# Optimization experiments

Hardware: AMD Instinct MI355X
Metric: run time of the kernel (lower is better)

## Reference

```python
import jax, jax.numpy as jnp
import numpy as np

IN_DIM = 128
HID = 128
OUT = 128

def _linear(x, W, b):
    return x @ W + b

def setup_inputs() -> dict:
    key = jax.random.key(0)
    ks = jax.random.split(key, 16)
    B, N = 2, 512
    def w(k, fan_in, fan_out):
        lim = 1.0 / np.sqrt(fan_in)
        return jax.random.uniform(k, (fan_in, fan_out), jnp.float32, -lim, lim)
    def bvec(k, fan_in, fan_out):
        lim = 1.0 / np.sqrt(fan_in)
        return jax.random.uniform(k, (fan_out,), jnp.float32, -lim, lim)
    return {
        "features": jax.random.normal(ks[0], (B, N, IN_DIM), jnp.float32),
        "coords": jax.random.normal(ks[1], (B, N, 3), jnp.float32),
        "eW1": w(ks[2], 2 * IN_DIM + 1, HID), "eb1": bvec(ks[3], 2 * IN_DIM + 1, HID),
        "eW2": w(ks[4], HID, HID), "eb2": bvec(ks[5], HID, HID),
        "nW1": w(ks[6], IN_DIM + HID, HID), "nb1": bvec(ks[7], IN_DIM + HID, HID),
        "nW2": w(ks[8], HID, OUT), "nb2": bvec(ks[9], HID, OUT),
        "cW1": w(ks[10], HID, HID), "cb1": bvec(ks[11], HID, HID),
        "cW2": w(ks[12], HID, 1), "cb2": bvec(ks[13], HID, 1),
    }

def reference(features, coords, eW1, eb1, eW2, eb2, nW1, nb1, nW2, nb2, cW1, cb1, cW2, cb2):
    B, N, D = features.shape
    # pairwise coordinate differences and distances: (B, N, N, 3), (B, N, N, 1)
    coord_diff = coords[:, :, None, :] - coords[:, None, :, :]
    distances = jnp.sqrt(jnp.sum(coord_diff ** 2, axis=-1, keepdims=True) + 1e-8)
    # all-pairs edge features: (B, N, N, 2D+1)
    feat_i = jnp.broadcast_to(features[:, :, None, :], (B, N, N, D))
    feat_j = jnp.broadcast_to(features[:, None, :, :], (B, N, N, D))
    edge_features = jnp.concatenate([feat_i, feat_j, distances], axis=-1)
    edge_hidden = _linear(jax.nn.silu(_linear(edge_features, eW1, eb1)), eW2, eb2)
    # mean over neighbors j -> (B, N, HID)
    aggregated = jnp.mean(edge_hidden, axis=2)
    node_input = jnp.concatenate([features, aggregated], axis=-1)
    updated_features = _linear(jax.nn.silu(_linear(node_input, nW1, nb1)), nW2, nb2)
    # coordinate update
    coord_weights = _linear(jax.nn.silu(_linear(edge_hidden, cW1, cb1)), cW2, cb2)  # (B,N,N,1)
    updated_coords = coords + jnp.mean(coord_weights * coord_diff, axis=2)
    return (updated_features, updated_coords)
```

## Files before the change

### kernel.cpp

```cpp
#include <hip/hip_runtime.h>
#include <hip/hip_bf16.h>
#include <math.h>


typedef float f32x4 __attribute__((ext_vector_type(4)));
typedef short short8 __attribute__((ext_vector_type(8)));

#define MFMA16(a, b, c) __builtin_amdgcn_mfma_f32_16x16x32_bf16((a), (b), (c), 0, 0, 0)

__device__ __forceinline__ short f2bf(float x) {
    __hip_bfloat16 h = __float2bfloat16(x);
    union { __hip_bfloat16 h; short s; } v; v.h = h;
    return v.s;
}
__device__ __forceinline__ float bf2f(short s) {
    union { unsigned u; float f; } v; v.u = ((unsigned)(unsigned short)s) << 16;
    return v.f;
}
__device__ __forceinline__ float silu_f(float x) {
    return x * __builtin_amdgcn_rcpf(1.0f + __expf(-x));
}

__device__ __forceinline__ int swz(int row, int col) {
    int byte = (row << 8) | (col << 1);
    byte ^= (row & 7) << 4;
    return byte >> 1;
}

__global__ void egnn_prew(const float* __restrict__ feat, const float* __restrict__ eW1,
                          const float* __restrict__ eb1,
                          const float* __restrict__ eW2, const float* __restrict__ cW1,
                          const float* __restrict__ eb2, const float* __restrict__ cb1,
                          float* __restrict__ Abuf, float* __restrict__ Bbuf,
                          unsigned short* __restrict__ MbfT, float* __restrict__ bias2ws,
                          float* __restrict__ aggpart, float* __restrict__ coordpart) {
    const int bid = blockIdx.x;
    const int t = threadIdx.x;
    if (bid < 1024) {
        __shared__ float f[128];
        if (t < 128) f[t] = feat[bid * 128 + t];
        __syncthreads();
        const int col  = t & 127;
        const int half = t >> 7;
        const float* W = eW1 + (size_t)half * 128 * 128 + col;
        float acc = half ? 0.f : eb1[col];
        #pragma unroll 8
        for (int k = 0; k < 128; ++k) acc += f[k] * W[(size_t)k * 128];
        if (half == 0) Abuf[bid * 128 + col] = acc;
        else           Bbuf[bid * 128 + col] = acc;
        if (t < 128) aggpart[(size_t)bid * 128 + t] = 0.f;
        if (t < 3)   coordpart[bid * 3 + t] = 0.f;
    } else {
        const int idx = (bid - 1024) * 2 + (t >> 7);
        const int c = t & 127;
        if (idx < 128) {
            float acc = 0.f;
            #pragma unroll 8
            for (int h = 0; h < 128; ++h) acc += eW2[idx * 128 + h] * cW1[h * 128 + c];
            MbfT[c * 128 + idx] = (unsigned short)f2bf(acc);
        } else if (idx == 128) {
            float acc = cb1[c];
            #pragma unroll 8
            for (int h = 0; h < 128; ++h) acc += eb2[h] * cW1[h * 128 + c];
            bias2ws[c] = acc;
        }
    }
}

__global__ void __launch_bounds__(256, 2) egnn_main(
    const float* __restrict__ coords, const float* __restrict__ eW1,
    const float* __restrict__ cW2, const float* __restrict__ cb2,
    const float* __restrict__ Abuf, const float* __restrict__ Bbuf,
    const unsigned short* __restrict__ MbfT, const float* __restrict__ bias2ws,
    float* __restrict__ aggpart, float* __restrict__ coordpart)
{
    constexpr int Nn = 512;
    __shared__ __align__(16) short se[64 * 128];
    __shared__ float aw[128], wd[128];
    __shared__ float cdp[2][3][64];
    __shared__ float warr[2][4][64];
    __shared__ float aggred[16][128];
    __shared__ float cred[4][3];
    __shared__ float ci3[3];

    const int tid  = threadIdx.x;
    const int lane = tid & 63;
    const int wave = tid >> 6;
    const int bid  = blockIdx.x;
    const int node = bid >> 2;
    const int quad = bid & 3;
    const int b    = node >> 9;

    if (tid < 128) {
        aw[tid] = Abuf[node * 128 + tid];
        wd[tid] = eW1[256 * 128 + tid];
    }
    if (tid == 0) {
        ci3[0] = coords[node * 3 + 0];
        ci3[1] = coords[node * 3 + 1];
        ci3[2] = coords[node * 3 + 2];
    }

    const int cfrag = wave * 32 + (lane & 15);
    const int koff  = (lane >> 4) * 8;
    short8 wfM[2][4];
    #pragma unroll
    for (int n2 = 0; n2 < 2; ++n2)
        #pragma unroll
        for (int k = 0; k < 4; ++k)
            wfM[n2][k] = *(const short8*)&MbfT[(size_t)(cfrag + n2 * 16) * 128 + k * 32 + koff];
    __syncthreads();

    const float b2_0  = bias2ws[cfrag], b2_1 = bias2ws[cfrag + 16];
    const float cw2_0 = cW2[cfrag],     cw2_1 = cW2[cfrag + 16];
    const float cb2v  = cb2[0];
    const float cix = ci3[0], ciy = ci3[1], ciz = ci3[2];

    const int jr = tid >> 2, cb = (tid & 3) * 32;
    const int rg = tid >> 4, c8 = (tid & 15) * 8;

    float ap[8];
    #pragma unroll
    for (int q = 0; q < 8; ++q) ap[q] = 0.f;
    float cax = 0.f, cay = 0.f, caz = 0.f;

    for (int t = 0; t < 2; ++t) {
        const int par = t & 1;
        {
            const int j = quad * 128 + t * 64 + jr;
            const float dx = cix - coords[(b * Nn + j) * 3 + 0];
            const float dy = ciy - coords[(b * Nn + j) * 3 + 1];
            const float dz = ciz - coords[(b * Nn + j) * 3 + 2];
            const float dj = sqrtf(dx * dx + dy * dy + dz * dz + 1e-8f);
            if ((tid & 3) == 0) {
                cdp[par][0][jr] = dx; cdp[par][1][jr] = dy; cdp[par][2][jr] = dz;
            }
            const float* Bj = Bbuf + (size_t)(b * Nn + j) * 128 + cb;
            #pragma unroll
            for (int cc = 0; cc < 32; cc += 8) {
                f32x4 x0 = *(const f32x4*)(Bj + cc);
                f32x4 x1 = *(const f32x4*)(Bj + cc + 4);
                short8 v;
                #pragma unroll
                for (int r = 0; r < 4; ++r) {
                    const int c = cb + cc + r;
                    v[r] = f2bf(silu_f(aw[c] + x0[r] + dj * wd[c]));
                }
                #pragma unroll
                for (int r = 0; r < 4; ++r) {
                    const int c = cb + cc + 4 + r;
                    v[4 + r] = f2bf(silu_f(aw[c] + x1[r] + dj * wd[c]));
                }
                *(short8*)&se[swz(jr, cb + cc)] = v;
            }
        }
        __syncthreads();

        f32x4 acc[4][2];
        #pragma unroll
        for (int m = 0; m < 4; ++m) {
            acc[m][0] = (f32x4){b2_0, b2_0, b2_0, b2_0};
            acc[m][1] = (f32x4){b2_1, b2_1, b2_1, b2_1};
        }
        #pragma unroll
        for (int m = 0; m < 4; ++m)
            #pragma unroll
            for (int k = 0; k < 4; ++k) {
                short8 a = *(const short8*)&se[swz(m * 16 + (lane & 15), k * 32 + koff)];
                acc[m][0] = MFMA16(a, wfM[0][k], acc[m][0]);
                acc[m][1] = MFMA16(a, wfM[1][k], acc[m][1]);
            }

        #pragma unroll
        for (int r = 0; r < 4; ++r) {
            short8 v = *(const short8*)&se[swz(rg * 4 + r, c8)];
            #pragma unroll
            for (int q = 0; q < 8; ++q) ap[q] += bf2f(v[q]);
        }

        #pragma unroll
        for (int m = 0; m < 4; ++m)
            #pragma unroll
            for (int reg = 0; reg < 4; ++reg) {
                float v = silu_f(acc[m][0][reg]) * cw2_0
                        + silu_f(acc[m][1][reg]) * cw2_1;
                v += __shfl_xor(v, 1); v += __shfl_xor(v, 2);
                v += __shfl_xor(v, 4); v += __shfl_xor(v, 8);
                if ((lane & 15) == 0)
                    warr[par][wave][m * 16 + (lane >> 4) * 4 + reg] = v;
            }
        __syncthreads();

        if (lane < 16) {
            const int row = wave * 16 + lane;
            const float w = warr[par][0][row] + warr[par][1][row]
                          + warr[par][2][row] + warr[par][3][row] + cb2v;
            cax += w * cdp[par][0][row];
            cay += w * cdp[par][1][row];
            caz += w * cdp[par][2][row];
        }
    }

    #pragma unroll
    for (int q = 0; q < 8; ++q) aggred[rg][c8 + q] = ap[q];
    {
        float sx = cax, sy = cay, sz = caz;
        sx += __shfl_xor(sx, 1); sy += __shfl_xor(sy, 1); sz += __shfl_xor(sz, 1);
        sx += __shfl_xor(sx, 2); sy += __shfl_xor(sy, 2); sz += __shfl_xor(sz, 2);
        sx += __shfl_xor(sx, 4); sy += __shfl_xor(sy, 4); sz += __shfl_xor(sz, 4);
        sx += __shfl_xor(sx, 8); sy += __shfl_xor(sy, 8); sz += __shfl_xor(sz, 8);
        if (lane == 0) { cred[wave][0] = sx; cred[wave][1] = sy; cred[wave][2] = sz; }
    }
    __syncthreads();
    if (tid < 128) {
        float s = 0.f;
        #pragma unroll
        for (int g = 0; g < 16; ++g) s += aggred[g][tid];
        atomicAdd(&aggpart[(size_t)node * 128 + tid], s);
    }
    if (tid < 3) {
        atomicAdd(&coordpart[node * 3 + tid],
                  cred[0][tid] + cred[1][tid] + cred[2][tid] + cred[3][tid]);
    }
}

__global__ void egnn_post(
    const float* __restrict__ features, const float* __restrict__ coords,
    const float* __restrict__ eW2, const float* __restrict__ eb2,
    const float* __restrict__ nW1, const float* __restrict__ nb1,
    const float* __restrict__ nW2, const float* __restrict__ nb2,
    const float* __restrict__ aggpart, const float* __restrict__ coordpart,
    float* __restrict__ out_feat, float* __restrict__ out_coord)
{
    __shared__ float aggs[128], aggh[128], hbuf[128], fi[128], part[128];
    const int node = blockIdx.x;
    const int tid  = threadIdx.x;
    const int c = tid & 127, g = tid >> 7;

    if (tid < 128) {
        aggs[tid] = aggpart[(size_t)node * 128 + tid];
        fi[tid]   = features[node * 128 + tid];
    }
    if (tid < 3)
        out_coord[node * 3 + tid] = coords[node * 3 + tid]
                                  + coordpart[node * 3 + tid] * (1.f / 512.f);
    __syncthreads();
    {
        float acc = 0.f;
        #pragma unroll 8
        for (int k = g * 64; k < g * 64 + 64; ++k) acc += aggs[k] * eW2[k * 128 + c];
        if (g == 1) part[c] = acc;
        __syncthreads();
        if (g == 0) aggh[c] = (acc + part[c]) * (1.f / 512.f) + eb2[c];
        __syncthreads();
    }
    {
        float acc = (g == 0) ? nb1[c] : 0.f;
        const float* src = (g == 0) ? fi : aggh;
        const float* W = nW1 + (size_t)(g << 7) * 128 + c;
        #pragma unroll 8
        for (int k = 0; k < 128; ++k) acc += src[k] * W[(size_t)k * 128];
        if (g == 1) part[c] = acc;
        __syncthreads();
        if (g == 0) hbuf[c] = silu_f(acc + part[c]);
        __syncthreads();
    }
    {
        float acc = (g == 0) ? nb2[c] : 0.f;
        #pragma unroll 8
        for (int k = g * 64; k < g * 64 + 64; ++k) acc += hbuf[k] * nW2[k * 128 + c];
        if (g == 1) part[c] = acc;
        __syncthreads();
        if (g == 0) out_feat[node * 128 + c] = acc + part[c];
    }
}

extern "C" void kernel_launch(void* const* d_in, const int* in_sizes, int n_in,
                              void* d_out, int out_size, void* d_ws, size_t ws_size,
                              hipStream_t stream)
{
    const float* features = (const float*)d_in[0];
    const float* coords   = (const float*)d_in[1];
    const float* eW1 = (const float*)d_in[2];
    const float* eb1 = (const float*)d_in[3];
    const float* eW2 = (const float*)d_in[4];
    const float* eb2 = (const float*)d_in[5];
    const float* nW1 = (const float*)d_in[6];
    const float* nb1 = (const float*)d_in[7];
    const float* nW2 = (const float*)d_in[8];
    const float* nb2 = (const float*)d_in[9];
    const float* cW1 = (const float*)d_in[10];
    const float* cb1 = (const float*)d_in[11];
    const float* cW2 = (const float*)d_in[12];
    const float* cb2 = (const float*)d_in[13];

    float* out = (float*)d_out;
    float* out_feat  = out;
    float* out_coord = out + 2 * 512 * 128;

    float* Abuf      = (float*)d_ws;
    float* Bbuf      = Abuf + 2 * 512 * 128;
    unsigned short* MbfT = (unsigned short*)(Bbuf + 2 * 512 * 128);
    float* bias2ws   = (float*)(MbfT + 128 * 128);
    float* aggpart   = bias2ws + 128;
    float* coordpart = aggpart + 1024 * 128;

    egnn_prew<<<1089, 256, 0, stream>>>(features, eW1, eb1, eW2, cW1, eb2, cb1,
                                        Abuf, Bbuf, MbfT, bias2ws, aggpart, coordpart);
    egnn_main<<<4096, 256, 0, stream>>>(coords, eW1, cW2, cb2,
                                        Abuf, Bbuf, MbfT, bias2ws,
                                        aggpart, coordpart);
    egnn_post<<<1024, 256, 0, stream>>>(features, coords, eW2, eb2,
                                        nW1, nb1, nW2, nb2,
                                        aggpart, coordpart, out_feat, out_coord);
}
```

Baseline: 184.9 us.

## Fuse node-update MLP into main kernel via last-block completion counter

Removes the separate post kernel. Each node is now split across two blocks instead of four, and each block handles 256 neighbours over four tiles. A per-node atomic counter picks the last finishing block, which then reads the accumulated partial sums and runs the node MLP and coordinate update. This saves one kernel launch and halves the number of atomic partial writes. In exchange it adds a threadfence and an atomic handshake, and the tail MLP work now runs unevenly inside the main kernel's blocks.

```diff
diff --git a/kernel.cpp b/kernel.cpp
--- a/kernel.cpp
+++ b/kernel.cpp
@@ -33,7 +33,8 @@
                           const float* __restrict__ eb2, const float* __restrict__ cb1,
                           float* __restrict__ Abuf, float* __restrict__ Bbuf,
                           unsigned short* __restrict__ MbfT, float* __restrict__ bias2ws,
-                          float* __restrict__ aggpart, float* __restrict__ coordpart) {
+                          float* __restrict__ aggpart, float* __restrict__ coordpart,
+                          int* __restrict__ done) {
     const int bid = blockIdx.x;
     const int t = threadIdx.x;
     if (bid < 1024) {
@@ -50,6 +51,7 @@
         else           Bbuf[bid * 128 + col] = acc;
         if (t < 128) aggpart[(size_t)bid * 128 + t] = 0.f;
         if (t < 3)   coordpart[bid * 3 + t] = 0.f;
+        if (t == 0)  done[bid] = 0;
     } else {
         const int idx = (bid - 1024) * 2 + (t >> 7);
         const int c = t & 127;
@@ -68,11 +70,17 @@
 }
 
 __global__ void __launch_bounds__(256, 2) egnn_main(
-    const float* __restrict__ coords, const float* __restrict__ eW1,
+    const float* __restrict__ features, const float* __restrict__ coords,
+    const float* __restrict__ eW1, const float* __restrict__ eW2,
+    const float* __restrict__ eb2,
+    const float* __restrict__ nW1, const float* __restrict__ nb1,
+    const float* __restrict__ nW2, const float* __restrict__ nb2,
     const float* __restrict__ cW2, const float* __restrict__ cb2,
     const float* __restrict__ Abuf, const float* __restrict__ Bbuf,
     const unsigned short* __restrict__ MbfT, const float* __restrict__ bias2ws,
-    float* __restrict__ aggpart, float* __restrict__ coordpart)
+    float* __restrict__ aggpart, float* __restrict__ coordpart,
+    int* __restrict__ done,
+    float* __restrict__ out_feat, float* __restrict__ out_coord)
 {
     constexpr int Nn = 512;
     __shared__ __align__(16) short se[64 * 128];
@@ -82,13 +90,15 @@
     __shared__ float aggred[16][128];
     __shared__ float cred[4][3];
     __shared__ float ci3[3];
+    __shared__ float pfi[128], paggh[128], phbuf[128], ppart[128], pcd[3];
+    __shared__ int lastflag;
 
     const int tid  = threadIdx.x;
     const int lane = tid & 63;
     const int wave = tid >> 6;
     const int bid  = blockIdx.x;
-    const int node = bid >> 2;
-    const int quad = bid & 3;
+    const int node = bid >> 1;
+    const int half = bid & 1;
     const int b    = node >> 9;
 
     if (tid < 128) {
@@ -124,10 +134,10 @@
     for (int q = 0; q < 8; ++q) ap[q] = 0.f;
     float cax = 0.f, cay = 0.f, caz = 0.f;
 
-    for (int t = 0; t < 2; ++t) {
+    for (int t = 0; t < 4; ++t) {
         const int par = t & 1;
         {
-            const int j = quad * 128 + t * 64 + jr;
+            const int j = half * 256 + t * 64 + jr;
             const float dx = cix - coords[(b * Nn + j) * 3 + 0];
             const float dy = ciy - coords[(b * Nn + j) * 3 + 1];
             const float dz = ciz - coords[(b * Nn + j) * 3 + 2];
@@ -222,56 +232,52 @@
         atomicAdd(&coordpart[node * 3 + tid],
                   cred[0][tid] + cred[1][tid] + cred[2][tid] + cred[3][tid]);
     }
-}
-
-__global__ void egnn_post(
-    const float* __restrict__ features, const float* __restrict__ coords,
-    const float* __restrict__ eW2, const float* __restrict__ eb2,
-    const float* __restrict__ nW1, const float* __restrict__ nb1,
-    const float* __restrict__ nW2, const float* __restrict__ nb2,
-    const float* __restrict__ aggpart, const float* __restrict__ coordpart,
-    float* __restrict__ out_feat, float* __restrict__ out_coord)
-{
-    __shared__ float aggs[128], aggh[128], hbuf[128], fi[128], part[128];
-    const int node = blockIdx.x;
-    const int tid  = threadIdx.x;
-    const int c = tid & 127, g = tid >> 7;
-
-    if (tid < 128) {
-        aggs[tid] = aggpart[(size_t)node * 128 + tid];
-        fi[tid]   = features[node * 128 + tid];
-    }
-    if (tid < 3)
-        out_coord[node * 3 + tid] = coords[node * 3 + tid]
-                                  + coordpart[node * 3 + tid] * (1.f / 512.f);
+    __threadfence();
     __syncthreads();
-    {
-        float acc = 0.f;
-        #pragma unroll 8
-        for (int k = g * 64; k < g * 64 + 64; ++k) acc += aggs[k] * eW2[k * 128 + c];
-        if (g == 1) part[c] = acc;
+    if (tid == 0)
+        lastflag = (__hip_atomic_fetch_add(&done[node], 1, __ATOMIC_ACQ_REL,
+                                           __HIP_MEMORY_SCOPE_AGENT) == 1) ? 1 : 0;
+    __syncthreads();
+
+    if (lastflag) {
+        const int c = tid & 127, g = tid >> 7;
+        if (tid < 128) {
+            ppart[tid] = atomicAdd(&aggpart[(size_t)node * 128 + tid], 0.f);
+            pfi[tid]   = features[node * 128 + tid];
+        }
+        if (tid < 3) pcd[tid] = atomicAdd(&coordpart[node * 3 + tid], 0.f);
         __syncthreads();
-        if (g == 0) aggh[c] = (acc + part[c]) * (1.f / 512.f) + eb2[c];
-        __syncthreads();
-    }
-    {
-        float acc = (g == 0) ? nb1[c] : 0.f;
-        const float* src = (g == 0) ? fi : aggh;
-        const float* W = nW1 + (size_t)(g << 7) * 128 + c;
-        #pragma unroll 8
-        for (int k = 0; k < 128; ++k) acc += src[k] * W[(size_t)k * 128];
-        if (g == 1) part[c] = acc;
-        __syncthreads();
-        if (g == 0) hbuf[c] = silu_f(acc + part[c]);
-        __syncthreads();
-    }
-    {
-        float acc = (g == 0) ? nb2[c] : 0.f;
-        #pragma unroll 8
-        for (int k = g * 64; k < g * 64 + 64; ++k) acc += hbuf[k] * nW2[k * 128 + c];
-        if (g == 1) part[c] = acc;
-        __syncthreads();
-        if (g == 0) out_feat[node * 128 + c] = acc + part[c];
+        if (tid < 3)
+            out_coord[node * 3 + tid] = ci3[tid] + pcd[tid] * (1.f / 512.f);
+        {
+            float acc2 = 0.f;
+            #pragma unroll 8
+            for (int k = g * 64; k < g * 64 + 64; ++k) acc2 += ppart[k] * eW2[k * 128 + c];
+            __syncthreads();
+            if (g == 1) phbuf[c] = acc2;
+            __syncthreads();
+            if (g == 0) paggh[c] = (acc2 + phbuf[c]) * (1.f / 512.f) + eb2[c];
+            __syncthreads();
+        }
+        {
+            float acc2 = (g == 0) ? nb1[c] : 0.f;
+            const float* src = (g == 0) ? pfi : paggh;
+            const float* W = nW1 + (size_t)(g << 7) * 128 + c;
+            #pragma unroll 8
+            for (int k = 0; k < 128; ++k) acc2 += src[k] * W[(size_t)k * 128];
+            if (g == 1) ppart[c] = acc2;
+            __syncthreads();
+            if (g == 0) phbuf[c] = silu_f(acc2 + ppart[c]);
+            __syncthreads();
+        }
+        {
+            float acc2 = (g == 0) ? nb2[c] : 0.f;
+            #pragma unroll 8
+            for (int k = g * 64; k < g * 64 + 64; ++k) acc2 += phbuf[k] * nW2[k * 128 + c];
+            if (g == 1) ppart[c] = acc2;
+            __syncthreads();
+            if (g == 0) out_feat[node * 128 + c] = acc2 + ppart[c];
+        }
     }
 }
 
@@ -304,13 +310,14 @@
     float* bias2ws   = (float*)(MbfT + 128 * 128);
     float* aggpart   = bias2ws + 128;
     float* coordpart = aggpart + 1024 * 128;
+    int*   done      = (int*)(coordpart + 1024 * 3);
 
     egnn_prew<<<1089, 256, 0, stream>>>(features, eW1, eb1, eW2, cW1, eb2, cb1,
-                                        Abuf, Bbuf, MbfT, bias2ws, aggpart, coordpart);
-    egnn_main<<<4096, 256, 0, stream>>>(coords, eW1, cW2, cb2,
                                         Abuf, Bbuf, MbfT, bias2ws,
-                                        aggpart, coordpart);
-    egnn_post<<<1024, 256, 0, stream>>>(features, coords, eW2, eb2,
-                                        nW1, nb1, nW2, nb2,
-                                        aggpart, coordpart, out_feat, out_coord);
-}
+                                        aggpart, coordpart, done);
+    egnn_main<<<2048, 256, 0, stream>>>(features, coords, eW1, eW2, eb2,
+                                        nW1, nb1, nW2, nb2, cW2, cb2,
+                                        Abuf, Bbuf, MbfT, bias2ws,
+                                        aggpart, coordpart, done,
+                                        out_feat, out_coord);
+}
```

New measurement: 322.0 us. 1.74x slower.
